# Performance work log

Measured on AMD Instinct MI355X. Metric: run time of the kernel, lower is better.

Reference implementation:

```python
import jax, jax.numpy as jnp
import numpy as np

N = 50000       # nodes
E = 800000      # edges (avg degree 16)
C_IN = 128
C_OUT = 128
RATIO = 0.5
K = int(np.ceil(RATIO * N))  # static top-k size (single graph)
EPS = 1e-5      # BatchNorm eps


def setup_inputs() -> dict:
    key = jax.random.key(0)
    ks = jax.random.split(key, 12)
    x = jax.random.normal(ks[0], (N, C_IN), jnp.float32)
    edge_index = jax.random.randint(ks[1], (2, E), 0, N, dtype=jnp.int32)
    batch = jnp.zeros((N,), jnp.int32)
    s_in = 1.0 / np.sqrt(C_IN)
    s_out = 1.0 / np.sqrt(C_OUT)
    return {
        "x": x,
        "edge_index": edge_index,
        "batch": batch,
        "lin_w": jax.random.uniform(ks[2], (C_IN, C_OUT), jnp.float32, -s_in, s_in),
        "lin_b": jax.random.uniform(ks[3], (C_OUT,), jnp.float32, -s_in, s_in),
        "bn1_g": jnp.ones((C_OUT,), jnp.float32),
        "bn1_b": jnp.zeros((C_OUT,), jnp.float32),
        "gcn_w": jax.random.uniform(ks[4], (C_OUT, C_OUT), jnp.float32, -s_out, s_out),
        "gcn_b": jnp.zeros((C_OUT,), jnp.float32),
        "bn2_g": jnp.ones((C_OUT,), jnp.float32),
        "bn2_b": jnp.zeros((C_OUT,), jnp.float32),
        "pool_w": jax.random.uniform(ks[5], (C_OUT,), jnp.float32, -s_out, s_out),
    }


def _batchnorm(h, g, b):
    # training-mode BatchNorm1d: biased variance over the node axis
    mu = jnp.mean(h, axis=0)
    var = jnp.mean(jnp.square(h - mu), axis=0)
    return (h - mu) * jax.lax.rsqrt(var + EPS) * g + b


def reference(x, edge_index, batch, lin_w, lin_b, bn1_g, bn1_b,
              gcn_w, gcn_b, bn2_g, bn2_b, pool_w):
    # ---- MLP: Linear + BN + ReLU ----
    h = jax.nn.relu(_batchnorm(x @ lin_w + lin_b, bn1_g, bn1_b))

    # ---- GCNConv with self-loops + symmetric normalization ----
    loops = jnp.arange(N, dtype=edge_index.dtype)
    row = jnp.concatenate([edge_index[0], loops])  # source
    col = jnp.concatenate([edge_index[1], loops])  # target
    hw = h @ gcn_w                                    # [N, C_OUT]
    deg = jax.ops.segment_sum(jnp.ones_like(col, jnp.float32), col, num_segments=N)
    dinv = jnp.where(deg > 0, jax.lax.rsqrt(deg), 0.0)
    norm = dinv[row] * dinv[col]                      # [E+N]
    agg = jax.ops.segment_sum(hw[row] * norm[:, None], col, num_segments=N)
    out = agg + gcn_b

    # ---- BN + ReLU ----
    h2 = jax.nn.relu(_batchnorm(out, bn2_g, bn2_b))

    # ---- TopKPooling (single graph -> static k) ----
    score = jnp.tanh((h2 @ pool_w) / jnp.linalg.norm(pool_w))
    top_score, perm = jax.lax.top_k(score, K)
    x_pool = h2[perm] * top_score[:, None]            # [K, C_OUT]
    batch_new = batch[perm]

    # filter_adj with fixed shape: dropped edges marked -1
    mask = jnp.zeros((N,), bool).at[perm].set(True)
    new_idx = jnp.full((N,), -1, edge_index.dtype).at[perm].set(
        jnp.arange(K, dtype=edge_index.dtype))
    src, dst = edge_index[0], edge_index[1]
    keep = mask[src] & mask[dst]
    ei_new = jnp.where(keep[None, :],
                       jnp.stack([new_idx[src], new_idx[dst]]),
                       jnp.array(-1, edge_index.dtype))
    return x_pool, ei_new, batch_new
```

## Files before the change

kernel.cpp:

```cpp
#include <hip/hip_runtime.h>
#include <hip/hip_bf16.h>

#define NN 50000
#define EE 800000
#define KTOP 25000
#define EPSF 1e-5
#define NB (1 << 18)
#define KSHIFT 14

__global__ __launch_bounds__(256, 2) void gemm_bn_stats(const float* __restrict__ A,
                                                        const float* __restrict__ W,
                                                        const float* __restrict__ bias,
                                                        float* __restrict__ Y,
                                                        double* __restrict__ part, int M) {
    __shared__ float Bs[128][128];
    __shared__ float As[32][132];
    int t = threadIdx.x;
    int bm = blockIdx.x * 128;

    const float4* W4 = (const float4*)W;
    float4* Bs4 = (float4*)Bs;
#pragma unroll
    for (int i = 0; i < 16; i++) Bs4[t + i * 256] = W4[t + i * 256];

    float acc[8][8];
#pragma unroll
    for (int i = 0; i < 8; i++)
#pragma unroll
        for (int j = 0; j < 8; j++) acc[i][j] = 0.f;

    int ty = t >> 4;
    int tx = t & 15;

    for (int kc = 0; kc < 4; kc++) {
        __syncthreads();
#pragma unroll
        for (int i = 0; i < 4; i++) {
            int f4 = t + i * 256;
            int r = f4 >> 3, k4 = f4 & 7;
            int row = bm + r;
            float4 v = make_float4(0.f, 0.f, 0.f, 0.f);
            if (row < M) v = *(const float4*)&A[(size_t)row * 128 + kc * 32 + k4 * 4];
            As[k4 * 4 + 0][r] = v.x;
            As[k4 * 4 + 1][r] = v.y;
            As[k4 * 4 + 2][r] = v.z;
            As[k4 * 4 + 3][r] = v.w;
        }
        __syncthreads();
#pragma unroll
        for (int kk = 0; kk < 32; kk++) {
            float4 a0 = *(float4*)&As[kk][ty * 8];
            float4 a1 = *(float4*)&As[kk][ty * 8 + 4];
            float4 b0 = *(float4*)&Bs[kc * 32 + kk][tx * 4];
            float4 b1 = *(float4*)&Bs[kc * 32 + kk][64 + tx * 4];
            float av[8] = {a0.x, a0.y, a0.z, a0.w, a1.x, a1.y, a1.z, a1.w};
            float bv[8] = {b0.x, b0.y, b0.z, b0.w, b1.x, b1.y, b1.z, b1.w};
#pragma unroll
            for (int i = 0; i < 8; i++)
#pragma unroll
                for (int j = 0; j < 8; j++) acc[i][j] += av[i] * bv[j];
        }
    }

    float4 bb0 = *(const float4*)&bias[tx * 4];
    float4 bb1 = *(const float4*)&bias[64 + tx * 4];
    float s[8], s2[8];
#pragma unroll
    for (int j = 0; j < 8; j++) { s[j] = 0.f; s2[j] = 0.f; }
#pragma unroll
    for (int i = 0; i < 8; i++) {
        int row = bm + ty * 8 + i;
        if (row < M) {
            float4 y0, y1;
            y0.x = acc[i][0] + bb0.x; y0.y = acc[i][1] + bb0.y;
            y0.z = acc[i][2] + bb0.z; y0.w = acc[i][3] + bb0.w;
            y1.x = acc[i][4] + bb1.x; y1.y = acc[i][5] + bb1.y;
            y1.z = acc[i][6] + bb1.z; y1.w = acc[i][7] + bb1.w;
            *(float4*)&Y[(size_t)row * 128 + tx * 4] = y0;
            *(float4*)&Y[(size_t)row * 128 + 64 + tx * 4] = y1;
            s[0] += y0.x; s2[0] += y0.x * y0.x;
            s[1] += y0.y; s2[1] += y0.y * y0.y;
            s[2] += y0.z; s2[2] += y0.z * y0.z;
            s[3] += y0.w; s2[3] += y0.w * y0.w;
            s[4] += y1.x; s2[4] += y1.x * y1.x;
            s[5] += y1.y; s2[5] += y1.y * y1.y;
            s[6] += y1.z; s2[6] += y1.z * y1.z;
            s[7] += y1.w; s2[7] += y1.w * y1.w;
        }
    }
    __syncthreads();
    float2* Sred = (float2*)As;
#pragma unroll
    for (int j = 0; j < 8; j++) {
        int col = (j < 4) ? (tx * 4 + j) : (64 + tx * 4 + j - 4);
        Sred[ty * 128 + col] = make_float2(s[j], s2[j]);
    }
    __syncthreads();
    if (t < 128) {
        double S = 0.0, S2 = 0.0;
#pragma unroll
        for (int r = 0; r < 16; r++) {
            float2 v = Sred[r * 128 + t];
            S += (double)v.x;
            S2 += (double)v.y;
        }
        part[((size_t)blockIdx.x * 128 + t) * 2 + 0] = S;
        part[((size_t)blockIdx.x * 128 + t) * 2 + 1] = S2;
    }
}

__global__ __launch_bounds__(256, 2) void gemm_bn_apply(const float* __restrict__ Yin,
                                                        const float* __restrict__ W,
                                                        const float* __restrict__ sc,
                                                        const float* __restrict__ sh,
                                                        const float* __restrict__ dinv,
                                                        float* __restrict__ HWs, int M) {
    __shared__ float Bs[128][128];
    __shared__ float As[32][132];
    int t = threadIdx.x;
    int bm = blockIdx.x * 128;

    const float4* W4 = (const float4*)W;
    float4* Bs4 = (float4*)Bs;
#pragma unroll
    for (int i = 0; i < 16; i++) Bs4[t + i * 256] = W4[t + i * 256];

    float acc[8][8];
#pragma unroll
    for (int i = 0; i < 8; i++)
#pragma unroll
        for (int j = 0; j < 8; j++) acc[i][j] = 0.f;

    int ty = t >> 4;
    int tx = t & 15;

    for (int kc = 0; kc < 4; kc++) {
        __syncthreads();
#pragma unroll
        for (int i = 0; i < 4; i++) {
            int f4 = t + i * 256;
            int r = f4 >> 3, k4 = f4 & 7;
            int row = bm + r;
            int col = kc * 32 + k4 * 4;
            float4 v = make_float4(0.f, 0.f, 0.f, 0.f);
            if (row < M) {
                float4 y = *(const float4*)&Yin[(size_t)row * 128 + col];
                float4 scv = *(const float4*)&sc[col];
                float4 shv = *(const float4*)&sh[col];
                v.x = fmaxf(y.x * scv.x + shv.x, 0.f);
                v.y = fmaxf(y.y * scv.y + shv.y, 0.f);
                v.z = fmaxf(y.z * scv.z + shv.z, 0.f);
                v.w = fmaxf(y.w * scv.w + shv.w, 0.f);
            }
            As[k4 * 4 + 0][r] = v.x;
            As[k4 * 4 + 1][r] = v.y;
            As[k4 * 4 + 2][r] = v.z;
            As[k4 * 4 + 3][r] = v.w;
        }
        __syncthreads();
#pragma unroll
        for (int kk = 0; kk < 32; kk++) {
            float4 a0 = *(float4*)&As[kk][ty * 8];
            float4 a1 = *(float4*)&As[kk][ty * 8 + 4];
            float4 b0 = *(float4*)&Bs[kc * 32 + kk][tx * 4];
            float4 b1 = *(float4*)&Bs[kc * 32 + kk][64 + tx * 4];
            float av[8] = {a0.x, a0.y, a0.z, a0.w, a1.x, a1.y, a1.z, a1.w};
            float bv[8] = {b0.x, b0.y, b0.z, b0.w, b1.x, b1.y, b1.z, b1.w};
#pragma unroll
            for (int i = 0; i < 8; i++)
#pragma unroll
                for (int j = 0; j < 8; j++) acc[i][j] += av[i] * bv[j];
        }
    }
#pragma unroll
    for (int i = 0; i < 8; i++) {
        int row = bm + ty * 8 + i;
        if (row < M) {
            float di = dinv[row];
            float4 o0, o1;
            o0.x = acc[i][0] * di; o0.y = acc[i][1] * di;
            o0.z = acc[i][2] * di; o0.w = acc[i][3] * di;
            o1.x = acc[i][4] * di; o1.y = acc[i][5] * di;
            o1.z = acc[i][6] * di; o1.w = acc[i][7] * di;
            *(float4*)&HWs[(size_t)row * 128 + tx * 4] = o0;
            *(float4*)&HWs[(size_t)row * 128 + 64 + tx * 4] = o1;
        }
    }
}

__global__ __launch_bounds__(256) void bn_finalize(const double* __restrict__ part, int nb,
                                                   const float* __restrict__ g,
                                                   const float* __restrict__ beta,
                                                   float* __restrict__ scale,
                                                   float* __restrict__ shift, int M) {
    int c = blockIdx.x;
    int t = threadIdx.x;
    double s = 0.0, s2 = 0.0;
    for (int b = t; b < nb; b += 256) {
        s += part[((size_t)b * 128 + c) * 2 + 0];
        s2 += part[((size_t)b * 128 + c) * 2 + 1];
    }
    __shared__ double sd[256], sd2[256];
    sd[t] = s;
    sd2[t] = s2;
    __syncthreads();
#pragma unroll
    for (int o = 128; o > 0; o >>= 1) {
        if (t < o) {
            sd[t] += sd[t + o];
            sd2[t] += sd2[t + o];
        }
        __syncthreads();
    }
    if (t == 0) {
        double S = sd[0], S2 = sd2[0];
        double mu = S / (double)M;
        double var = S2 / (double)M - mu * mu;
        double inv = 1.0 / sqrt(var + (double)EPSF);
        scale[c] = (float)((double)g[c] * inv);
        shift[c] = (float)((double)beta[c] - mu * (double)g[c] * inv);
    }
}

__global__ __launch_bounds__(256) void bn_finalize2(const float2* __restrict__ part, int nb,
                                                    const float* __restrict__ g,
                                                    const float* __restrict__ beta,
                                                    float* __restrict__ scale,
                                                    float* __restrict__ shift, int M) {
    int c = blockIdx.x;
    int t = threadIdx.x;
    double s = 0.0, s2 = 0.0;
    for (int b = t; b < nb; b += 256) {
        float2 v = part[(size_t)b * 128 + c];
        s += (double)v.x;
        s2 += (double)v.y;
    }
    __shared__ double sd[256], sd2[256];
    sd[t] = s;
    sd2[t] = s2;
    __syncthreads();
#pragma unroll
    for (int o = 128; o > 0; o >>= 1) {
        if (t < o) {
            sd[t] += sd[t + o];
            sd2[t] += sd2[t + o];
        }
        __syncthreads();
    }
    if (t == 0) {
        double S = sd[0], S2 = sd2[0];
        double mu = S / (double)M;
        double var = S2 / (double)M - mu * mu;
        double inv = 1.0 / sqrt(var + (double)EPSF);
        scale[c] = (float)((double)g[c] * inv);
        shift[c] = (float)((double)beta[c] - mu * (double)g[c] * inv);
    }
}

__global__ __launch_bounds__(256) void count_deg(const int* __restrict__ col,
                                                 int* __restrict__ cnt,
                                                 int* __restrict__ zbase, int zn, int E) {
    int e = blockIdx.x * 256 + threadIdx.x;
    if (e < zn) zbase[e] = 0;
    if (e < E) atomicAdd(&cnt[col[e]], 1);
}

__global__ __launch_bounds__(256) void fill_csr(const int* __restrict__ row,
                                                const int* __restrict__ col,
                                                const int* __restrict__ off,
                                                int* __restrict__ cur,
                                                int* __restrict__ csr, int E) {
    int e = blockIdx.x * 256 + threadIdx.x;
    if (e < E) {
        int c = col[e];
        int p = atomicAdd(&cur[c], 1);
        csr[off[c] + p] = row[e];
    }
}

__device__ __forceinline__ int waveInclScan(int v, int lane) {
#pragma unroll
    for (int o = 1; o < 64; o <<= 1) {
        int u = __shfl_up(v, o, 64);
        if (lane >= o) v += u;
    }
    return v;
}

__global__ __launch_bounds__(1024) void scan_phase1(const int* __restrict__ in,
                                                    int* __restrict__ out,
                                                    int* __restrict__ bsum,
                                                    float* __restrict__ dinv, int n) {
    int t = threadIdx.x;
    int g = blockIdx.x * 1024 + t;
    int lane = t & 63, wid = t >> 6;
    int v = (g < n) ? in[g] : 0;
    if (dinv && g < n) dinv[g] = (float)(1.0 / sqrt((double)(v + 1)));
    int incl = waveInclScan(v, lane);
    __shared__ int ws[16];
    if (lane == 63) ws[wid] = incl;
    __syncthreads();
    if (t < 16) {
        int x = ws[t];
#pragma unroll
        for (int o = 1; o < 16; o <<= 1) {
            int u = __shfl_up(x, o, 64);
            if (t >= o) x += u;
        }
        ws[t] = x;
    }
    __syncthreads();
    int pre = (wid > 0) ? ws[wid - 1] : 0;
    if (g < n) out[g] = pre + incl - v;
    if (t == 1023) bsum[blockIdx.x] = ws[15];
}

__global__ __launch_bounds__(1024) void scan_phase23(const int* __restrict__ bsum, int B,
                                                     int* __restrict__ out, int n) {
    int t = threadIdx.x;
    int lane = t & 63, wid = t >> 6;
    int v = (t < B) ? bsum[t] : 0;
    int incl = waveInclScan(v, lane);
    __shared__ int ws[16];
    if (lane == 63) ws[wid] = incl;
    __syncthreads();
    if (t < 16) {
        int x = ws[t];
#pragma unroll
        for (int o = 1; o < 16; o <<= 1) {
            int u = __shfl_up(x, o, 64);
            if (t >= o) x += u;
        }
        ws[t] = x;
    }
    __syncthreads();
    int pre = (wid > 0) ? ws[wid - 1] : 0;
    __shared__ int sb[1024];
    if (t < B) sb[t] = pre + incl - v;
    if (t == B - 1) out[n] = pre + incl;
    __syncthreads();
    for (int idx = t; idx < n; idx += 1024) out[idx] += sb[idx >> 10];
}

__global__ __launch_bounds__(512) void gcn_agg(const float* __restrict__ HWs,
                                               const int* __restrict__ off,
                                               const int* __restrict__ csr,
                                               const float* __restrict__ dinv,
                                               const float* __restrict__ gcn_b,
                                               float* __restrict__ OUT,
                                               float2* __restrict__ part32, int M) {
    int t = threadIdx.x;
    int w = t >> 6;
    int lane = t & 63;
    int half = lane >> 5;
    int l32 = lane & 31;
    int i = blockIdx.x * 8 + w;

    const float4* H4 = (const float4*)HWs;
    double a0 = 0.0, a1 = 0.0, a2 = 0.0, a3 = 0.0;

    if (i < M) {
        int o0 = off[i], o1 = off[i + 1];
        if (half == 0) {
            float4 sv = H4[(size_t)i * 32 + l32];
            a0 = sv.x; a1 = sv.y; a2 = sv.z; a3 = sv.w;
        }
        int e = o0;
        for (; e + 4 <= o1; e += 4) {
            int sA = csr[e + half];
            int sB = csr[e + 2 + half];
            float4 vA = H4[(size_t)sA * 32 + l32];
            float4 vB = H4[(size_t)sB * 32 + l32];
            a0 += (double)vA.x + (double)vB.x;
            a1 += (double)vA.y + (double)vB.y;
            a2 += (double)vA.z + (double)vB.z;
            a3 += (double)vA.w + (double)vB.w;
        }
        if (e + 2 <= o1) {
            int sA = csr[e + half];
            float4 vA = H4[(size_t)sA * 32 + l32];
            a0 += (double)vA.x; a1 += (double)vA.y;
            a2 += (double)vA.z; a3 += (double)vA.w;
            e += 2;
        }
        if (e < o1 && half == 0) {
            int sA = csr[e];
            float4 vA = H4[(size_t)sA * 32 + l32];
            a0 += (double)vA.x; a1 += (double)vA.y;
            a2 += (double)vA.z; a3 += (double)vA.w;
        }
    }
    a0 += __shfl_down(a0, 32, 64);
    a1 += __shfl_down(a1, 32, 64);
    a2 += __shfl_down(a2, 32, 64);
    a3 += __shfl_down(a3, 32, 64);

    __shared__ float4 sredS[8][32];
    __shared__ float4 sredQ[8][32];
    if (half == 0) {
        if (i < M) {
            double di = (double)dinv[i];
            float4 gb = ((const float4*)gcn_b)[l32];
            float4 y;
            y.x = (float)(a0 * di) + gb.x;
            y.y = (float)(a1 * di) + gb.y;
            y.z = (float)(a2 * di) + gb.z;
            y.w = (float)(a3 * di) + gb.w;
            ((float4*)OUT)[(size_t)i * 32 + l32] = y;
            sredS[w][l32] = y;
            sredQ[w][l32] = make_float4(y.x * y.x, y.y * y.y, y.z * y.z, y.w * y.w);
        } else {
            sredS[w][l32] = make_float4(0.f, 0.f, 0.f, 0.f);
            sredQ[w][l32] = make_float4(0.f, 0.f, 0.f, 0.f);
        }
    }
    __syncthreads();
    if (t < 128) {
        const float* fS = (const float*)sredS;
        const float* fQ = (const float*)sredQ;
        float S = 0.f, S2 = 0.f;
#pragma unroll
        for (int ww = 0; ww < 8; ww++) {
            S += fS[ww * 128 + t];
            S2 += fQ[ww * 128 + t];
        }
        part32[(size_t)blockIdx.x * 128 + t] = make_float2(S, S2);
    }
}

__global__ __launch_bounds__(256) void score_key(const float* __restrict__ Y2,
                                                 const float* __restrict__ sc,
                                                 const float* __restrict__ sh,
                                                 const float* __restrict__ w,
                                                 float* __restrict__ score,
                                                 unsigned* __restrict__ key,
                                                 int* __restrict__ bcnt, int M) {
    int lane = threadIdx.x & 63;
    int wid = threadIdx.x >> 6;
    int gw = blockIdx.x * 4 + wid;
    int nw = gridDim.x * 4;

    float w0 = w[lane], w1 = w[lane + 64];
    float sc0 = sc[lane], sh0 = sh[lane];
    float sc1 = sc[lane + 64], sh1 = sh[lane + 64];

    float nv = w0 * w0 + w1 * w1;
#pragma unroll
    for (int o = 32; o >= 1; o >>= 1) nv += __shfl_xor(nv, o, 64);
    float nrm = sqrtf(nv);

    for (int r = gw; r < M; r += nw) {
        float a = Y2[(size_t)r * 128 + lane];
        float b = Y2[(size_t)r * 128 + lane + 64];
        a = fmaxf(a * sc0 + sh0, 0.f);
        b = fmaxf(b * sc1 + sh1, 0.f);
        float v = a * w0 + b * w1;
#pragma unroll
        for (int o = 32; o >= 1; o >>= 1) v += __shfl_xor(v, o, 64);
        if (lane == 0) {
            score[r] = tanhf(v / nrm);
            unsigned u = __float_as_uint(v);
            unsigned k = (u & 0x80000000u) ? ~u : (u | 0x80000000u);
            key[r] = k;
            atomicAdd(&bcnt[k >> KSHIFT], 1);
        }
    }
}

__global__ __launch_bounds__(256) void bucket_fill(const unsigned* __restrict__ key,
                                                   const int* __restrict__ boff,
                                                   int* __restrict__ bcur,
                                                   uint2* __restrict__ bmem, int M) {
    int i = blockIdx.x * 256 + threadIdx.x;
    if (i < M) {
        unsigned k = key[i];
        int b = k >> KSHIFT;
        int p = atomicAdd(&bcur[b], 1);
        bmem[boff[b] + p] = make_uint2(k, (unsigned)i);
    }
}

__global__ __launch_bounds__(256) void rank_kernel(const unsigned* __restrict__ key,
                                                   const int* __restrict__ boff,
                                                   const uint2* __restrict__ bmem,
                                                   int* __restrict__ rank,
                                                   int* __restrict__ nidx, int M) {
    int i = blockIdx.x * 256 + threadIdx.x;
    if (i >= M) return;
    unsigned ki = key[i];
    int b = ki >> KSHIFT;
    int r = M - boff[b + 1];
    int p0 = boff[b], p1 = boff[b + 1];
    for (int p = p0; p < p1; p++) {
        uint2 kj = bmem[p];
        if (kj.x > ki || (kj.x == ki && (int)kj.y < i)) r++;
    }
    rank[i] = r;
    nidx[i] = (r < KTOP) ? r : -1;
}

#define MPB ((NN + 7) / 8)
#define EB ((EE + 255) / 256)

__global__ __launch_bounds__(256) void write_all(const float* __restrict__ Y2,
                                                 const float* __restrict__ sc,
                                                 const float* __restrict__ sh,
                                                 const float* __restrict__ score,
                                                 const int* __restrict__ rank,
                                                 const int* __restrict__ erow,
                                                 const int* __restrict__ ecol,
                                                 const int* __restrict__ nidx,
                                                 float* __restrict__ out0,
                                                 float* __restrict__ out1,
                                                 float* __restrict__ out2, int M, int E) {
    int blk = blockIdx.x;
    if (blk < MPB) {
        int sub = threadIdx.x >> 5;
        int c4 = threadIdx.x & 31;
        int i = blk * 8 + sub;
        if (i >= M) return;
        int r = rank[i];
        if (r < KTOP) {
            float s = score[i];
            float4 y = *(const float4*)&Y2[(size_t)i * 128 + c4 * 4];
            float4 scv = *(const float4*)&sc[c4 * 4];
            float4 shv = *(const float4*)&sh[c4 * 4];
            float4 o;
            o.x = fmaxf(y.x * scv.x + shv.x, 0.f) * s;
            o.y = fmaxf(y.y * scv.y + shv.y, 0.f) * s;
            o.z = fmaxf(y.z * scv.z + shv.z, 0.f) * s;
            o.w = fmaxf(y.w * scv.w + shv.w, 0.f) * s;
            *(float4*)&out0[(size_t)r * 128 + c4 * 4] = o;
            if (c4 == 0) out2[r] = 0.0f;
        }
    } else {
        int e = (blk - MPB) * 256 + threadIdx.x;
        if (e < E) {
            int a = nidx[erow[e]];
            int b = nidx[ecol[e]];
            bool keep = (a >= 0) && (b >= 0);
            out1[e] = keep ? (float)a : -1.0f;
            out1[E + e] = keep ? (float)b : -1.0f;
        }
    }
}

extern "C" void kernel_launch(void* const* d_in, const int* in_sizes, int n_in,
                              void* d_out, int out_size, void* d_ws, size_t ws_size,
                              hipStream_t stream) {
    const float* x = (const float*)d_in[0];
    const int* ei = (const int*)d_in[1];
    const float* lin_w = (const float*)d_in[3];
    const float* lin_b = (const float*)d_in[4];
    const float* bn1_g = (const float*)d_in[5];
    const float* bn1_b = (const float*)d_in[6];
    const float* gcn_w = (const float*)d_in[7];
    const float* gcn_b = (const float*)d_in[8];
    const float* bn2_g = (const float*)d_in[9];
    const float* bn2_b = (const float*)d_in[10];
    const float* pool_w = (const float*)d_in[11];

    const int* e_row = ei;
    const int* e_col = ei + EE;

    char* ws = (char*)d_ws;
    size_t off_b = 0;
    auto alloc = [&](size_t bytes) -> void* {
        void* p = ws + off_b;
        off_b = (off_b + bytes + 255) & ~(size_t)255;
        return p;
    };
    float* y = (float*)alloc((size_t)NN * 128 * 4);
    float* hws = (float*)alloc((size_t)NN * 128 * 4);
    int* cnt = (int*)alloc(NN * 4);
    int* cur = (int*)alloc(NN * 4);
    int* offs = (int*)alloc((NN + 1) * 4);
    float* dinv = (float*)alloc(NN * 4);
    int* csr = (int*)alloc((size_t)EE * 4);
    float* score = (float*)alloc(NN * 4);
    unsigned* key = (unsigned*)alloc(NN * 4);
    int* rank = (int*)alloc(NN * 4);
    int* nidx = (int*)alloc(NN * 4);
    int* bcnt = (int*)alloc((size_t)NB * 4);
    int* bcur = (int*)alloc((size_t)NB * 4);
    int* boff = (int*)alloc(((size_t)NB + 1) * 4);
    uint2* bmem = (uint2*)alloc((size_t)NN * 8);
    double* part = (double*)alloc((size_t)400 * 128 * 2 * 8);
    float* scale1 = (float*)alloc(128 * 4);
    float* shift1 = (float*)alloc(128 * 4);
    float* scale2 = (float*)alloc(128 * 4);
    float* shift2 = (float*)alloc(128 * 4);
    int* bsum = (int*)alloc(256 * 4);

    float* out0 = (float*)d_out;
    float* out1 = out0 + (size_t)KTOP * 128;
    float* out2 = out1 + (size_t)2 * EE;

    float2* part32 = (float2*)out0;
    int gcn_grid = (NN + 7) / 8;
    int gemm_grid = (NN + 127) / 128;

    hipMemsetAsync(cnt, 0, (size_t)((char*)cur - (char*)cnt) + NN * 4, stream);
    count_deg<<<(EE + 255) / 256, 256, 0, stream>>>(e_col, cnt, bcnt, 2 * NB, EE);
    {
        int B = (NN + 1023) / 1024;
        scan_phase1<<<B, 1024, 0, stream>>>(cnt, offs, bsum, dinv, NN);
        scan_phase23<<<1, 1024, 0, stream>>>(bsum, B, offs, NN);
    }
    fill_csr<<<(EE + 255) / 256, 256, 0, stream>>>(e_row, e_col, offs, cur, csr, EE);

    gemm_bn_stats<<<gemm_grid, 256, 0, stream>>>(x, lin_w, lin_b, y, part, NN);
    bn_finalize<<<128, 256, 0, stream>>>(part, gemm_grid, bn1_g, bn1_b, scale1, shift1, NN);

    gemm_bn_apply<<<gemm_grid, 256, 0, stream>>>(y, gcn_w, scale1, shift1, dinv, hws, NN);
    gcn_agg<<<gcn_grid, 512, 0, stream>>>(hws, offs, csr, dinv, gcn_b, y, part32, NN);

    bn_finalize2<<<128, 256, 0, stream>>>(part32, gcn_grid, bn2_g, bn2_b, scale2, shift2, NN);

    score_key<<<512, 256, 0, stream>>>(y, scale2, shift2, pool_w, score, key, bcnt, NN);
    {
        int B = NB / 1024;
        scan_phase1<<<B, 1024, 0, stream>>>(bcnt, boff, bsum, nullptr, NB);
        scan_phase23<<<1, 1024, 0, stream>>>(bsum, B, boff, NB);
    }
    bucket_fill<<<(NN + 255) / 256, 256, 0, stream>>>(key, boff, bcur, bmem, NN);
    rank_kernel<<<(NN + 255) / 256, 256, 0, stream>>>(key, boff, bmem, rank, nidx, NN);

    write_all<<<MPB + EB, 256, 0, stream>>>(y, scale2, shift2, score, rank,
                                            e_row, e_col, nidx, out0, out1, out2, NN, EE);
}
```

Baseline: 370.9 us.

## Fold scan block offsets into consumers, fuse rank with pooling, shrink bucket count

The second scan pass no longer adds block prefixes back into the offset arrays. Instead, consumers (fill_csr, gcn_agg, bucket_fill, rank) add the per-1024-block prefix when they read an offset, which removes a serial full-array update in a single-block kernel. The top-k rank computation is fused with the pooled-feature write, so the rank array is no longer stored and reloaded, and edge filtering becomes its own kernel. The bucket count drops from 2^18 to 2^16, which cuts the scan and zeroing work but puts more keys in each bucket for the linear rank loop.

New measurement: 378.8 us. +2.1%, slower.

```diff
diff --git a/kernel.cpp b/kernel.cpp
--- a/kernel.cpp
+++ b/kernel.cpp
@@ -5,8 +5,8 @@
 #define EE 800000
 #define KTOP 25000
 #define EPSF 1e-5
-#define NB (1 << 18)
-#define KSHIFT 14
+#define NB 65536
+#define KSHIFT 16
 
 __global__ __launch_bounds__(256, 2) void gemm_bn_stats(const float* __restrict__ A,
                                                         const float* __restrict__ W,
@@ -268,13 +268,14 @@
 __global__ __launch_bounds__(256) void fill_csr(const int* __restrict__ row,
                                                 const int* __restrict__ col,
                                                 const int* __restrict__ off,
+                                                const int* __restrict__ bsum,
                                                 int* __restrict__ cur,
                                                 int* __restrict__ csr, int E) {
     int e = blockIdx.x * 256 + threadIdx.x;
     if (e < E) {
         int c = col[e];
         int p = atomicAdd(&cur[c], 1);
-        csr[off[c] + p] = row[e];
+        csr[off[c] + bsum[c >> 10] + p] = row[e];
     }
 }
 
@@ -315,8 +316,7 @@
     if (t == 1023) bsum[blockIdx.x] = ws[15];
 }
 
-__global__ __launch_bounds__(1024) void scan_phase23(const int* __restrict__ bsum, int B,
-                                                     int* __restrict__ out, int n) {
+__global__ __launch_bounds__(1024) void scan_phase2(int* __restrict__ bsum, int B) {
     int t = threadIdx.x;
     int lane = t & 63, wid = t >> 6;
     int v = (t < B) ? bsum[t] : 0;
@@ -335,15 +335,12 @@
     }
     __syncthreads();
     int pre = (wid > 0) ? ws[wid - 1] : 0;
-    __shared__ int sb[1024];
-    if (t < B) sb[t] = pre + incl - v;
-    if (t == B - 1) out[n] = pre + incl;
-    __syncthreads();
-    for (int idx = t; idx < n; idx += 1024) out[idx] += sb[idx >> 10];
+    if (t < B) bsum[t] = pre + incl - v;
 }
 
 __global__ __launch_bounds__(512) void gcn_agg(const float* __restrict__ HWs,
                                                const int* __restrict__ off,
+                                               const int* __restrict__ bsum,
                                                const int* __restrict__ csr,
                                                const float* __restrict__ dinv,
                                                const float* __restrict__ gcn_b,
@@ -360,7 +357,8 @@
     double a0 = 0.0, a1 = 0.0, a2 = 0.0, a3 = 0.0;
 
     if (i < M) {
-        int o0 = off[i], o1 = off[i + 1];
+        int o0 = off[i] + bsum[i >> 10];
+        int o1 = (i + 1 < M) ? (off[i + 1] + bsum[(i + 1) >> 10]) : EE;
         if (half == 0) {
             float4 sv = H4[(size_t)i * 32 + l32];
             a0 = sv.x; a1 = sv.y; a2 = sv.z; a3 = sv.w;
@@ -469,6 +467,7 @@
 
 __global__ __launch_bounds__(256) void bucket_fill(const unsigned* __restrict__ key,
                                                    const int* __restrict__ boff,
+                                                   const int* __restrict__ bsum,
                                                    int* __restrict__ bcur,
                                                    uint2* __restrict__ bmem, int M) {
     int i = blockIdx.x * 256 + threadIdx.x;
@@ -476,72 +475,78 @@
         unsigned k = key[i];
         int b = k >> KSHIFT;
         int p = atomicAdd(&bcur[b], 1);
-        bmem[boff[b] + p] = make_uint2(k, (unsigned)i);
-    }
-}
-
-__global__ __launch_bounds__(256) void rank_kernel(const unsigned* __restrict__ key,
-                                                   const int* __restrict__ boff,
-                                                   const uint2* __restrict__ bmem,
-                                                   int* __restrict__ rank,
-                                                   int* __restrict__ nidx, int M) {
-    int i = blockIdx.x * 256 + threadIdx.x;
-    if (i >= M) return;
-    unsigned ki = key[i];
-    int b = ki >> KSHIFT;
-    int r = M - boff[b + 1];
-    int p0 = boff[b], p1 = boff[b + 1];
-    for (int p = p0; p < p1; p++) {
-        uint2 kj = bmem[p];
-        if (kj.x > ki || (kj.x == ki && (int)kj.y < i)) r++;
-    }
-    rank[i] = r;
-    nidx[i] = (r < KTOP) ? r : -1;
-}
-
-#define MPB ((NN + 7) / 8)
-#define EB ((EE + 255) / 256)
-
-__global__ __launch_bounds__(256) void write_all(const float* __restrict__ Y2,
+        bmem[boff[b] + bsum[b >> 10] + p] = make_uint2(k, (unsigned)i);
+    }
+}
+
+__global__ __launch_bounds__(256) void rank_pool(const unsigned* __restrict__ key,
+                                                 const int* __restrict__ boff,
+                                                 const int* __restrict__ bsum,
+                                                 const uint2* __restrict__ bmem,
+                                                 const float* __restrict__ Y2,
                                                  const float* __restrict__ sc,
                                                  const float* __restrict__ sh,
                                                  const float* __restrict__ score,
-                                                 const int* __restrict__ rank,
-                                                 const int* __restrict__ erow,
-                                                 const int* __restrict__ ecol,
-                                                 const int* __restrict__ nidx,
+                                                 int* __restrict__ nidx,
                                                  float* __restrict__ out0,
-                                                 float* __restrict__ out1,
-                                                 float* __restrict__ out2, int M, int E) {
-    int blk = blockIdx.x;
-    if (blk < MPB) {
-        int sub = threadIdx.x >> 5;
-        int c4 = threadIdx.x & 31;
-        int i = blk * 8 + sub;
-        if (i >= M) return;
-        int r = rank[i];
-        if (r < KTOP) {
-            float s = score[i];
-            float4 y = *(const float4*)&Y2[(size_t)i * 128 + c4 * 4];
-            float4 scv = *(const float4*)&sc[c4 * 4];
-            float4 shv = *(const float4*)&sh[c4 * 4];
-            float4 o;
-            o.x = fmaxf(y.x * scv.x + shv.x, 0.f) * s;
-            o.y = fmaxf(y.y * scv.y + shv.y, 0.f) * s;
-            o.z = fmaxf(y.z * scv.z + shv.z, 0.f) * s;
-            o.w = fmaxf(y.w * scv.w + shv.w, 0.f) * s;
-            *(float4*)&out0[(size_t)r * 128 + c4 * 4] = o;
-            if (c4 == 0) out2[r] = 0.0f;
-        }
-    } else {
-        int e = (blk - MPB) * 256 + threadIdx.x;
-        if (e < E) {
-            int a = nidx[erow[e]];
-            int b = nidx[ecol[e]];
-            bool keep = (a >= 0) && (b >= 0);
-            out1[e] = keep ? (float)a : -1.0f;
-            out1[E + e] = keep ? (float)b : -1.0f;
-        }
+                                                 float* __restrict__ out2, int M) {
+    __shared__ int lrank[256];
+    __shared__ float lscore[256];
+    int t = threadIdx.x;
+    int base = blockIdx.x * 256;
+    int i = base + t;
+    int r = 0x7fffffff;
+    if (i < M) {
+        unsigned ki = key[i];
+        int b = ki >> KSHIFT;
+        int p0 = boff[b] + bsum[b >> 10];
+        int p1 = (b + 1 < NB) ? (boff[b + 1] + bsum[(b + 1) >> 10]) : M;
+        r = M - p1;
+        for (int p = p0; p < p1; p++) {
+            uint2 kj = bmem[p];
+            if (kj.x > ki || (kj.x == ki && (int)kj.y < i)) r++;
+        }
+        nidx[i] = (r < KTOP) ? r : -1;
+        lscore[t] = score[i];
+    }
+    lrank[t] = r;
+    __syncthreads();
+
+    int sub = t >> 5;
+    int c4 = t & 31;
+    float4 scv = *(const float4*)&sc[c4 * 4];
+    float4 shv = *(const float4*)&sh[c4 * 4];
+    for (int n0 = 0; n0 < 256; n0 += 8) {
+        int li = n0 + sub;
+        int node = base + li;
+        if (node < M) {
+            int rr = lrank[li];
+            if (rr < KTOP) {
+                float s = lscore[li];
+                float4 y = *(const float4*)&Y2[(size_t)node * 128 + c4 * 4];
+                float4 o;
+                o.x = fmaxf(y.x * scv.x + shv.x, 0.f) * s;
+                o.y = fmaxf(y.y * scv.y + shv.y, 0.f) * s;
+                o.z = fmaxf(y.z * scv.z + shv.z, 0.f) * s;
+                o.w = fmaxf(y.w * scv.w + shv.w, 0.f) * s;
+                *(float4*)&out0[(size_t)rr * 128 + c4 * 4] = o;
+                if (c4 == 0) out2[rr] = 0.0f;
+            }
+        }
+    }
+}
+
+__global__ __launch_bounds__(256) void write_edges(const int* __restrict__ row,
+                                                   const int* __restrict__ col,
+                                                   const int* __restrict__ nidx,
+                                                   float* __restrict__ out1, int E) {
+    int e = blockIdx.x * 256 + threadIdx.x;
+    if (e < E) {
+        int a = nidx[row[e]];
+        int b = nidx[col[e]];
+        bool keep = (a >= 0) && (b >= 0);
+        out1[e] = keep ? (float)a : -1.0f;
+        out1[E + e] = keep ? (float)b : -1.0f;
     }
 }
 
@@ -579,7 +584,6 @@
     int* csr = (int*)alloc((size_t)EE * 4);
     float* score = (float*)alloc(NN * 4);
     unsigned* key = (unsigned*)alloc(NN * 4);
-    int* rank = (int*)alloc(NN * 4);
     int* nidx = (int*)alloc(NN * 4);
     int* bcnt = (int*)alloc((size_t)NB * 4);
     int* bcur = (int*)alloc((size_t)NB * 4);
@@ -590,7 +594,8 @@
     float* shift1 = (float*)alloc(128 * 4);
     float* scale2 = (float*)alloc(128 * 4);
     float* shift2 = (float*)alloc(128 * 4);
-    int* bsum = (int*)alloc(256 * 4);
+    int* bsumA = (int*)alloc(256 * 4);
+    int* bsumB = (int*)alloc(256 * 4);
 
     float* out0 = (float*)d_out;
     float* out1 = out0 + (size_t)KTOP * 128;
@@ -604,28 +609,27 @@
     count_deg<<<(EE + 255) / 256, 256, 0, stream>>>(e_col, cnt, bcnt, 2 * NB, EE);
     {
         int B = (NN + 1023) / 1024;
-        scan_phase1<<<B, 1024, 0, stream>>>(cnt, offs, bsum, dinv, NN);
-        scan_phase23<<<1, 1024, 0, stream>>>(bsum, B, offs, NN);
-    }
-    fill_csr<<<(EE + 255) / 256, 256, 0, stream>>>(e_row, e_col, offs, cur, csr, EE);
+        scan_phase1<<<B, 1024, 0, stream>>>(cnt, offs, bsumA, dinv, NN);
+        scan_phase2<<<1, 1024, 0, stream>>>(bsumA, B);
+    }
+    fill_csr<<<(EE + 255) / 256, 256, 0, stream>>>(e_row, e_col, offs, bsumA, cur, csr, EE);
 
     gemm_bn_stats<<<gemm_grid, 256, 0, stream>>>(x, lin_w, lin_b, y, part, NN);
     bn_finalize<<<128, 256, 0, stream>>>(part, gemm_grid, bn1_g, bn1_b, scale1, shift1, NN);
 
     gemm_bn_apply<<<gemm_grid, 256, 0, stream>>>(y, gcn_w, scale1, shift1, dinv, hws, NN);
-    gcn_agg<<<gcn_grid, 512, 0, stream>>>(hws, offs, csr, dinv, gcn_b, y, part32, NN);
+    gcn_agg<<<gcn_grid, 512, 0, stream>>>(hws, offs, bsumA, csr, dinv, gcn_b, y, part32, NN);
 
     bn_finalize2<<<128, 256, 0, stream>>>(part32, gcn_grid, bn2_g, bn2_b, scale2, shift2, NN);
 
     score_key<<<512, 256, 0, stream>>>(y, scale2, shift2, pool_w, score, key, bcnt, NN);
     {
         int B = NB / 1024;
-        scan_phase1<<<B, 1024, 0, stream>>>(bcnt, boff, bsum, nullptr, NB);
-        scan_phase23<<<1, 1024, 0, stream>>>(bsum, B, boff, NB);
-    }
-    bucket_fill<<<(NN + 255) / 256, 256, 0, stream>>>(key, boff, bcur, bmem, NN);
-    rank_kernel<<<(NN + 255) / 256, 256, 0, stream>>>(key, boff, bmem, rank, nidx, NN);
-
-    write_all<<<MPB + EB, 256, 0, stream>>>(y, scale2, shift2, score, rank,
-                                            e_row, e_col, nidx, out0, out1, out2, NN, EE);
-}
+        scan_phase1<<<B, 1024, 0, stream>>>(bcnt, boff, bsumB, nullptr, NB);
+        scan_phase2<<<1, 1024, 0, stream>>>(bsumB, B);
+    }
+    bucket_fill<<<(NN + 255) / 256, 256, 0, stream>>>(key, boff, bsumB, bcur, bmem, NN);
+    rank_pool<<<(NN + 255) / 256, 256, 0, stream>>>(key, boff, bsumB, bmem, y, scale2,
+                                                    shift2, score, nidx, out0, out2, NN);
+    write_edges<<<(EE + 255) / 256, 256, 0, stream>>>(e_row, e_col, nidx, out1, EE);
+}
```
